# Kernel tuning notes

Hardware: AMD Instinct MI355X
Metric: run time of the kernel (lower is better)

The kernel has to match this reference:

```python
import jax, jax.numpy as jnp
import numpy as np

EMBED_DIM = 1024
HEAD_DIM = 64
B, S = 16, 2048


def setup_inputs() -> dict:
    key = jax.random.key(0)
    ks = jax.random.split(key, 8)
    scale = 1.0 / np.sqrt(EMBED_DIM)
    return {
        "x": jax.random.normal(ks[0], (B, S, EMBED_DIM), dtype=jnp.float32),
        "mask": jax.random.randint(ks[1], (B, S), 0, 2, dtype=jnp.int32),
        "Wq": jax.random.normal(ks[2], (EMBED_DIM, HEAD_DIM), dtype=jnp.float32) * scale,
        "bq": jnp.zeros((HEAD_DIM,), dtype=jnp.float32),
        "Wk": jax.random.normal(ks[3], (EMBED_DIM, HEAD_DIM), dtype=jnp.float32) * scale,
        "bk": jnp.zeros((HEAD_DIM,), dtype=jnp.float32),
        "Wv": jax.random.normal(ks[4], (EMBED_DIM, HEAD_DIM), dtype=jnp.float32) * scale,
        "bv": jnp.zeros((HEAD_DIM,), dtype=jnp.float32),
    }


def reference(x, mask, Wq, bq, Wk, bk, Wv, bv):
    # x: [B,S,E], mask: [B,S] with 0 = masked, 1 = keep
    q = x @ Wq + bq          # [B,S,D]
    k = x @ Wk + bk          # [B,S,D]
    v = x @ Wv + bv          # [B,S,D]
    scores = jnp.einsum("bsd,btd->bst", q, k) / jnp.sqrt(jnp.float32(HEAD_DIM))
    scores = jnp.where(mask[:, None, :] == 0, jnp.float32(-1e9), scores)
    attn = jax.nn.softmax(scores, axis=-1)  # [B,S,S]
    return jnp.einsum("bst,btd->bsd", attn, v)  # [B,S,D]
```

## Files before the change

### kernel.cpp

```cpp
#include <hip/hip_runtime.h>
#include <math.h>

#define EMBED 1024
#define HDIM  64
#define BATCH 16
#define SEQ   2048
#define MTOT  (BATCH*SEQ)
#define NE    (MTOT*HDIM)

typedef _Float16 f16;
typedef __attribute__((ext_vector_type(8))) _Float16 half8;
typedef __attribute__((ext_vector_type(4))) _Float16 half4;
typedef __attribute__((ext_vector_type(4))) float  float4v;

__global__ void wprep_kernel(const float* __restrict__ Wq, const float* __restrict__ Wk,
                             const float* __restrict__ Wv, f16* __restrict__ Wt)
{
    int e = blockIdx.x * 256 + threadIdx.x;
    if (e >= 192 * EMBED) return;
    int gn = e >> 10, k = e & 1023;
    int mat = gn >> 6, n = gn & 63;
    const float* W = (mat == 0) ? Wq : ((mat == 1) ? Wk : Wv);
    Wt[e] = (f16)W[k * HDIM + n];
}

__global__ __launch_bounds__(256)
void qkv_mfma_kernel(const float* __restrict__ X, const f16* __restrict__ Wt,
                     const float* __restrict__ bq, const float* __restrict__ bk, const float* __restrict__ bv,
                     f16* __restrict__ Q, f16* __restrict__ K, f16* __restrict__ Vt)
{
    __shared__ f16 Xs[64 * 72];
    __shared__ f16 Csv[64 * 72];

    const int tid  = threadIdx.x;
    const int wave = tid >> 6;
    const int lane = tid & 63;
    const int quad = lane >> 4;
    const int c16  = lane & 15;
    const int m0   = blockIdx.x * 64;
    const int gnb  = wave * 3;

    float4v acc[4][3];
    #pragma unroll
    for (int mt = 0; mt < 4; ++mt)
        #pragma unroll
        for (int nt = 0; nt < 3; ++nt)
            acc[mt][nt] = (float4v){0.f, 0.f, 0.f, 0.f};

    float4 pf[4];
    #pragma unroll
    for (int i = 0; i < 4; ++i) {
        int c = tid + 256 * i, m = c >> 4, ko = (c & 15) * 4;
        pf[i] = *(const float4*)(X + (size_t)(m0 + m) * EMBED + ko);
    }

    for (int k0 = 0; k0 < EMBED; k0 += 64) {
        half8 bh[2][3];
        #pragma unroll
        for (int ks = 0; ks < 2; ++ks)
            #pragma unroll
            for (int nt = 0; nt < 3; ++nt)
                bh[ks][nt] = *(const half8*)(Wt + (size_t)((gnb + nt) * 16 + c16) * EMBED
                                             + k0 + ks * 32 + quad * 8);

        __syncthreads();
        #pragma unroll
        for (int i = 0; i < 4; ++i) {
            int c = tid + 256 * i, m = c >> 4, ko = (c & 15) * 4;
            half4 h = { (f16)pf[i].x, (f16)pf[i].y, (f16)pf[i].z, (f16)pf[i].w };
            *(half4*)&Xs[m * 72 + ko] = h;
        }
        __syncthreads();

        {
            int k1 = (k0 + 64) & (EMBED - 1);
            #pragma unroll
            for (int i = 0; i < 4; ++i) {
                int c = tid + 256 * i, m = c >> 4, ko = (c & 15) * 4;
                pf[i] = *(const float4*)(X + (size_t)(m0 + m) * EMBED + k1 + ko);
            }
        }

        #pragma unroll
        for (int ks = 0; ks < 2; ++ks) {
            half8 a[4];
            #pragma unroll
            for (int mt = 0; mt < 4; ++mt)
                a[mt] = *(const half8*)&Xs[(mt * 16 + c16) * 72 + ks * 32 + quad * 8];
            #pragma unroll
            for (int mt = 0; mt < 4; ++mt)
                #pragma unroll
                for (int nt = 0; nt < 3; ++nt)
                    acc[mt][nt] = __builtin_amdgcn_mfma_f32_16x16x32_f16(a[mt], bh[ks][nt], acc[mt][nt], 0, 0, 0);
        }
    }

    float bb[3];
    #pragma unroll
    for (int nt = 0; nt < 3; ++nt) {
        int gn = (gnb + nt) * 16 + c16, mat = gn >> 6, cn = gn & 63;
        bb[nt] = ((mat == 0) ? bq : ((mat == 1) ? bk : bv))[cn];
    }

    #pragma unroll
    for (int mt = 0; mt < 4; ++mt)
        #pragma unroll
        for (int nt = 0; nt < 3; ++nt) {
            int gn = (gnb + nt) * 16 + c16, mat = gn >> 6, cn = gn & 63;
            if (mat < 2) {
                f16* O = mat ? K : Q;
                #pragma unroll
                for (int r = 0; r < 4; ++r)
                    O[(size_t)(m0 + mt * 16 + quad * 4 + r) * HDIM + cn] =
                        (f16)(acc[mt][nt][r] + bb[nt]);
            }
        }

    __syncthreads();
    #pragma unroll
    for (int mt = 0; mt < 4; ++mt)
        #pragma unroll
        for (int nt = 0; nt < 3; ++nt) {
            int gn = (gnb + nt) * 16 + c16, mat = gn >> 6, cn = gn & 63;
            if (mat == 2) {
                #pragma unroll
                for (int r = 0; r < 4; ++r)
                    Csv[cn * 72 + mt * 16 + quad * 4 + r] = (f16)(acc[mt][nt][r] + bb[nt]);
            }
        }
    __syncthreads();
    {
        int d = tid >> 2, ms = (tid & 3) * 16;
        #pragma unroll
        for (int j = 0; j < 2; ++j)
            *(half8*)(Vt + (size_t)d * MTOT + m0 + ms + 8 * j) =
                *(const half8*)&Csv[d * 72 + ms + 8 * j];
    }
}

__global__ __launch_bounds__(256)
void attn_mfma_kernel(const f16* __restrict__ Q, const f16* __restrict__ K,
                      const f16* __restrict__ Vt, const int* __restrict__ mask,
                      float* __restrict__ out)
{
    __shared__ f16 Ks[64 * 72];
    __shared__ f16 Vs[64 * 72];
    __shared__ f16 Ps[4 * 16 * 72];
    __shared__ int maskS[64];

    const int tid  = threadIdx.x;
    const int wave = tid >> 6;
    const int lane = tid & 63;
    const int quad = lane >> 4;
    const int c16  = lane & 15;
    const int b    = blockIdx.y;
    const int s0   = blockIdx.x * 64;
    const int q0   = s0 + wave * 16;

    const size_t qrow = (size_t)(b * SEQ + q0 + c16) * HDIM;
    half8 qa0 = *(const half8*)(Q + qrow + quad * 8);
    half8 qa1 = *(const half8*)(Q + qrow + 32 + quad * 8);

    const half8 ones = { (f16)1.f, (f16)1.f, (f16)1.f, (f16)1.f,
                         (f16)1.f, (f16)1.f, (f16)1.f, (f16)1.f };

    float4v O[4];
    #pragma unroll
    for (int dt = 0; dt < 4; ++dt) O[dt] = (float4v){0.f, 0.f, 0.f, 0.f};
    float4v lacc = (float4v){0.f, 0.f, 0.f, 0.f};

    const size_t kbase = (size_t)b * SEQ * HDIM;
    const int vcol0 = b * SEQ;
    const int pbase = wave * 16 * 72;

    half8 pfK[2], pfV[2];
    int mreg;
    #pragma unroll
    for (int i = 0; i < 2; ++i) {
        int c = tid + 256 * i, j = c >> 3, o = (c & 7) * 8;
        pfK[i] = *(const half8*)(K  + kbase + (size_t)j * HDIM + o);
        pfV[i] = *(const half8*)(Vt + (size_t)j * MTOT + vcol0 + o);
    }
    mreg = mask[b * SEQ + (tid & 63)];

    for (int t0 = 0; t0 < SEQ; t0 += 64) {
        __syncthreads();
        #pragma unroll
        for (int i = 0; i < 2; ++i) {
            int c = tid + 256 * i, j = c >> 3, o = (c & 7) * 8;
            *(half8*)&Ks[j * 72 + o] = pfK[i];
            *(half8*)&Vs[j * 72 + o] = pfV[i];
        }
        if (tid < 64) maskS[tid] = mreg;
        __syncthreads();

        {
            int t1 = (t0 + 64) & (SEQ - 1);
            #pragma unroll
            for (int i = 0; i < 2; ++i) {
                int c = tid + 256 * i, j = c >> 3, o = (c & 7) * 8;
                pfK[i] = *(const half8*)(K  + kbase + (size_t)(t1 + j) * HDIM + o);
                pfV[i] = *(const half8*)(Vt + (size_t)j * MTOT + vcol0 + t1 + o);
            }
            mreg = mask[b * SEQ + t1 + (tid & 63)];
        }

        float4v s[4];
        #pragma unroll
        for (int nt = 0; nt < 4; ++nt) {
            const int krow = (nt * 16 + c16) * 72;
            half8 kh0 = *(const half8*)&Ks[krow + quad * 8];
            half8 kh1 = *(const half8*)&Ks[krow + 32 + quad * 8];
            float4v a = (float4v){0.f, 0.f, 0.f, 0.f};
            a = __builtin_amdgcn_mfma_f32_16x16x32_f16(qa0, kh0, a, 0, 0, 0);
            a = __builtin_amdgcn_mfma_f32_16x16x32_f16(qa1, kh1, a, 0, 0, 0);
            s[nt] = a;
        }

        #pragma unroll
        for (int nt = 0; nt < 4; ++nt) {
            int mk = maskS[nt * 16 + c16];
            #pragma unroll
            for (int r = 0; r < 4; ++r) {
                float t = fmaf(s[nt][r], 0.125f, -6.0f);
                t = mk ? t : -1e30f;
                Ps[pbase + (quad * 4 + r) * 72 + nt * 16 + c16] = (f16)__expf(t);
            }
        }

        const int prow = pbase + c16 * 72;
        half8 pa0 = *(const half8*)&Ps[prow + quad * 8];
        half8 pa1 = *(const half8*)&Ps[prow + 32 + quad * 8];
        lacc = __builtin_amdgcn_mfma_f32_16x16x32_f16(pa0, ones, lacc, 0, 0, 0);
        lacc = __builtin_amdgcn_mfma_f32_16x16x32_f16(pa1, ones, lacc, 0, 0, 0);
        #pragma unroll
        for (int dt = 0; dt < 4; ++dt) {
            const int vrow = (dt * 16 + c16) * 72;
            half8 vh0 = *(const half8*)&Vs[vrow + quad * 8];
            half8 vh1 = *(const half8*)&Vs[vrow + 32 + quad * 8];
            O[dt] = __builtin_amdgcn_mfma_f32_16x16x32_f16(pa0, vh0, O[dt], 0, 0, 0);
            O[dt] = __builtin_amdgcn_mfma_f32_16x16x32_f16(pa1, vh1, O[dt], 0, 0, 0);
        }
    }

    #pragma unroll
    for (int r = 0; r < 4; ++r) {
        float inv = 1.0f / lacc[r];
        size_t orow = (size_t)(b * SEQ + q0 + quad * 4 + r) * HDIM;
        #pragma unroll
        for (int dt = 0; dt < 4; ++dt)
            out[orow + dt * 16 + c16] = O[dt][r] * inv;
    }
}

extern "C" void kernel_launch(void* const* d_in, const int* in_sizes, int n_in,
                              void* d_out, int out_size, void* d_ws, size_t ws_size,
                              hipStream_t stream) {
    const float* x    = (const float*)d_in[0];
    const int*   mask = (const int*)  d_in[1];
    const float* Wq   = (const float*)d_in[2];
    const float* bq   = (const float*)d_in[3];
    const float* Wk   = (const float*)d_in[4];
    const float* bk   = (const float*)d_in[5];
    const float* Wv   = (const float*)d_in[6];
    const float* bv   = (const float*)d_in[7];
    float* out = (float*)d_out;

    f16* Qf = (f16*)d_ws;
    f16* Kf = Qf + (size_t)NE;
    f16* Vt = Kf + (size_t)NE;
    f16* Wt = Vt + (size_t)NE;

    wprep_kernel<<<dim3(768), dim3(256), 0, stream>>>(Wq, Wk, Wv, Wt);

    qkv_mfma_kernel<<<dim3(MTOT / 64), dim3(256), 0, stream>>>(
        x, Wt, bq, bk, bv, Qf, Kf, Vt);

    attn_mfma_kernel<<<dim3(SEQ / 64, BATCH), dim3(256), 0, stream>>>(
        Qf, Kf, Vt, mask, out);
}
```

Baseline: 261.6 us.

## Store K/V in MFMA fragment layout, split KV across blocks, add combine pass

The QKV kernel now writes K and V directly in per-lane MFMA fragment order, so the attention kernel loads operands straight from global memory into registers and no longer stages them through LDS with barriers. The X tile in the projection is double-buffered with a two-stage register prefetch, which drops one barrier per step. Attention splits the key range in two along a new grid dimension, and a new combine kernel sums the unnormalized partials and divides by the summed denominators. The exp is computed with exp2f using a pre-scaled constant. In exchange there is an extra launch plus fp32 partial-output traffic, and the attention kernel relies on global and L2 latency instead of shared-memory reuse.

```diff
diff --git a/kernel.cpp b/kernel.cpp
--- a/kernel.cpp
+++ b/kernel.cpp
@@ -27,9 +27,9 @@
 __global__ __launch_bounds__(256)
 void qkv_mfma_kernel(const float* __restrict__ X, const f16* __restrict__ Wt,
                      const float* __restrict__ bq, const float* __restrict__ bk, const float* __restrict__ bv,
-                     f16* __restrict__ Q, f16* __restrict__ K, f16* __restrict__ Vt)
-{
-    __shared__ f16 Xs[64 * 72];
+                     f16* __restrict__ Q, f16* __restrict__ Kf, f16* __restrict__ Vf)
+{
+    __shared__ f16 Xs[2][64 * 72];
     __shared__ f16 Csv[64 * 72];
 
     const int tid  = threadIdx.x;
@@ -47,53 +47,58 @@
         for (int nt = 0; nt < 3; ++nt)
             acc[mt][nt] = (float4v){0.f, 0.f, 0.f, 0.f};
 
-    float4 pf[4];
+    float4 pfA[4], pfB[4];
     #pragma unroll
     for (int i = 0; i < 4; ++i) {
         int c = tid + 256 * i, m = c >> 4, ko = (c & 15) * 4;
-        pf[i] = *(const float4*)(X + (size_t)(m0 + m) * EMBED + ko);
-    }
-
-    for (int k0 = 0; k0 < EMBED; k0 += 64) {
-        half8 bh[2][3];
-        #pragma unroll
-        for (int ks = 0; ks < 2; ++ks)
-            #pragma unroll
-            for (int nt = 0; nt < 3; ++nt)
-                bh[ks][nt] = *(const half8*)(Wt + (size_t)((gnb + nt) * 16 + c16) * EMBED
-                                             + k0 + ks * 32 + quad * 8);
-
-        __syncthreads();
-        #pragma unroll
-        for (int i = 0; i < 4; ++i) {
-            int c = tid + 256 * i, m = c >> 4, ko = (c & 15) * 4;
-            half4 h = { (f16)pf[i].x, (f16)pf[i].y, (f16)pf[i].z, (f16)pf[i].w };
-            *(half4*)&Xs[m * 72 + ko] = h;
-        }
-        __syncthreads();
-
-        {
-            int k1 = (k0 + 64) & (EMBED - 1);
-            #pragma unroll
-            for (int i = 0; i < 4; ++i) {
-                int c = tid + 256 * i, m = c >> 4, ko = (c & 15) * 4;
-                pf[i] = *(const float4*)(X + (size_t)(m0 + m) * EMBED + k1 + ko);
-            }
-        }
-
-        #pragma unroll
-        for (int ks = 0; ks < 2; ++ks) {
-            half8 a[4];
-            #pragma unroll
-            for (int mt = 0; mt < 4; ++mt)
-                a[mt] = *(const half8*)&Xs[(mt * 16 + c16) * 72 + ks * 32 + quad * 8];
-            #pragma unroll
-            for (int mt = 0; mt < 4; ++mt)
-                #pragma unroll
-                for (int nt = 0; nt < 3; ++nt)
-                    acc[mt][nt] = __builtin_amdgcn_mfma_f32_16x16x32_f16(a[mt], bh[ks][nt], acc[mt][nt], 0, 0, 0);
-        }
-    }
+        pfA[i] = *(const float4*)(X + (size_t)(m0 + m) * EMBED + ko);
+        pfB[i] = *(const float4*)(X + (size_t)(m0 + m) * EMBED + 64 + ko);
+    }
+
+#define QKV_STEP(PF, BUF, T)                                                      \
+    {                                                                             \
+        const int k0s = (T) * 64;                                                 \
+        half8 bh[2][3];                                                           \
+        _Pragma("unroll")                                                         \
+        for (int ks = 0; ks < 2; ++ks)                                            \
+            _Pragma("unroll")                                                     \
+            for (int nt = 0; nt < 3; ++nt)                                        \
+                bh[ks][nt] = *(const half8*)(Wt + (size_t)((gnb + nt) * 16 + c16) * EMBED \
+                                             + k0s + ks * 32 + quad * 8);         \
+        _Pragma("unroll")                                                         \
+        for (int i = 0; i < 4; ++i) {                                             \
+            int c = tid + 256 * i, m = c >> 4, ko = (c & 15) * 4;                 \
+            half4 h = { (f16)PF[i].x, (f16)PF[i].y, (f16)PF[i].z, (f16)PF[i].w }; \
+            *(half4*)&Xs[BUF][m * 72 + ko] = h;                                   \
+        }                                                                         \
+        __syncthreads();                                                          \
+        {                                                                         \
+            int k2 = (((T) + 2) & 15) * 64;                                       \
+            _Pragma("unroll")                                                     \
+            for (int i = 0; i < 4; ++i) {                                         \
+                int c = tid + 256 * i, m = c >> 4, ko = (c & 15) * 4;             \
+                PF[i] = *(const float4*)(X + (size_t)(m0 + m) * EMBED + k2 + ko); \
+            }                                                                     \
+        }                                                                         \
+        _Pragma("unroll")                                                         \
+        for (int ks = 0; ks < 2; ++ks) {                                          \
+            half8 a[4];                                                           \
+            _Pragma("unroll")                                                     \
+            for (int mt = 0; mt < 4; ++mt)                                        \
+                a[mt] = *(const half8*)&Xs[BUF][(mt * 16 + c16) * 72 + ks * 32 + quad * 8]; \
+            _Pragma("unroll")                                                     \
+            for (int mt = 0; mt < 4; ++mt)                                        \
+                _Pragma("unroll")                                                 \
+                for (int nt = 0; nt < 3; ++nt)                                    \
+                    acc[mt][nt] = __builtin_amdgcn_mfma_f32_16x16x32_f16(a[mt], bh[ks][nt], acc[mt][nt], 0, 0, 0); \
+        }                                                                         \
+    }
+
+    for (int t = 0; t < 16; t += 2) {
+        QKV_STEP(pfA, 0, t)
+        QKV_STEP(pfB, 1, t + 1)
+    }
+#undef QKV_STEP
 
     float bb[3];
     #pragma unroll
@@ -107,12 +112,20 @@
         #pragma unroll
         for (int nt = 0; nt < 3; ++nt) {
             int gn = (gnb + nt) * 16 + c16, mat = gn >> 6, cn = gn & 63;
-            if (mat < 2) {
-                f16* O = mat ? K : Q;
+            if (mat == 0) {
                 #pragma unroll
                 for (int r = 0; r < 4; ++r)
-                    O[(size_t)(m0 + mt * 16 + quad * 4 + r) * HDIM + cn] =
+                    Q[(size_t)(m0 + mt * 16 + quad * 4 + r) * HDIM + cn] =
                         (f16)(acc[mt][nt][r] + bb[nt]);
+            } else if (mat == 1) {
+                int ks = cn >> 5, q2 = (cn >> 3) & 3, dd = cn & 7;
+                int jt = (m0 >> 4) + mt;
+                #pragma unroll
+                for (int r = 0; r < 4; ++r) {
+                    int lanep = q2 * 16 + (quad * 4 + r);
+                    int idx = (jt * 2 + ks) * 512 + lanep * 8 + dd;
+                    Kf[idx] = (f16)(acc[mt][nt][r] + bb[nt]);
+                }
             }
         }
 
@@ -130,23 +143,26 @@
         }
     __syncthreads();
     {
-        int d = tid >> 2, ms = (tid & 3) * 16;
-        #pragma unroll
-        for (int j = 0; j < 2; ++j)
-            *(half8*)(Vt + (size_t)d * MTOT + m0 + ms + 8 * j) =
-                *(const half8*)&Csv[d * 72 + ms + 8 * j];
+        int c   = tid >> 5;
+        int s2  = tid & 31;
+        int jvl = c >> 2, dt = c & 3;
+        int fragg = ((m0 >> 5) + jvl) * 4 + dt;
+        #pragma unroll
+        for (int sub = 0; sub < 2; ++sub) {
+            int lp = s2 * 2 + sub;
+            int qp = lp >> 4, cp = lp & 15;
+            half8 v = *(const half8*)&Csv[(dt * 16 + cp) * 72 + jvl * 32 + qp * 8];
+            *(half8*)(Vf + (size_t)fragg * 512 + lp * 8) = v;
+        }
     }
 }
 
 __global__ __launch_bounds__(256)
-void attn_mfma_kernel(const f16* __restrict__ Q, const f16* __restrict__ K,
-                      const f16* __restrict__ Vt, const int* __restrict__ mask,
-                      float* __restrict__ out)
-{
-    __shared__ f16 Ks[64 * 72];
-    __shared__ f16 Vs[64 * 72];
+void attn_mfma_kernel(const f16* __restrict__ Q, const f16* __restrict__ Kf,
+                      const f16* __restrict__ Vf, const int* __restrict__ mask,
+                      float* __restrict__ Opart, float* __restrict__ lpart)
+{
     __shared__ f16 Ps[4 * 16 * 72];
-    __shared__ int maskS[64];
 
     const int tid  = threadIdx.x;
     const int wave = tid >> 6;
@@ -154,8 +170,8 @@
     const int quad = lane >> 4;
     const int c16  = lane & 15;
     const int b    = blockIdx.y;
-    const int s0   = blockIdx.x * 64;
-    const int q0   = s0 + wave * 16;
+    const int kvh  = blockIdx.z;
+    const int q0   = blockIdx.x * 64 + wave * 16;
 
     const size_t qrow = (size_t)(b * SEQ + q0 + c16) * HDIM;
     half8 qa0 = *(const half8*)(Q + qrow + quad * 8);
@@ -169,88 +185,80 @@
     for (int dt = 0; dt < 4; ++dt) O[dt] = (float4v){0.f, 0.f, 0.f, 0.f};
     float4v lacc = (float4v){0.f, 0.f, 0.f, 0.f};
 
-    const size_t kbase = (size_t)b * SEQ * HDIM;
-    const int vcol0 = b * SEQ;
     const int pbase = wave * 16 * 72;
-
-    half8 pfK[2], pfV[2];
-    int mreg;
-    #pragma unroll
-    for (int i = 0; i < 2; ++i) {
-        int c = tid + 256 * i, j = c >> 3, o = (c & 7) * 8;
-        pfK[i] = *(const half8*)(K  + kbase + (size_t)j * HDIM + o);
-        pfV[i] = *(const half8*)(Vt + (size_t)j * MTOT + vcol0 + o);
-    }
-    mreg = mask[b * SEQ + (tid & 63)];
-
-    for (int t0 = 0; t0 < SEQ; t0 += 64) {
-        __syncthreads();
-        #pragma unroll
-        for (int i = 0; i < 2; ++i) {
-            int c = tid + 256 * i, j = c >> 3, o = (c & 7) * 8;
-            *(half8*)&Ks[j * 72 + o] = pfK[i];
-            *(half8*)&Vs[j * 72 + o] = pfV[i];
-        }
-        if (tid < 64) maskS[tid] = mreg;
-        __syncthreads();
-
-        {
-            int t1 = (t0 + 64) & (SEQ - 1);
+    const int prow  = pbase + c16 * 72;
+    const int t_beg = kvh * (SEQ / 2);
+    const int t_end = t_beg + (SEQ / 2);
+
+    for (int t0 = t_beg; t0 < t_end; t0 += 64) {
+        const size_t fb = (size_t)(b * SEQ + t0) * 64;
+
+        float4v s[4];
+        #pragma unroll
+        for (int nt = 0; nt < 4; ++nt) {
+            half8 k0 = *(const half8*)(Kf + fb + nt * 1024 + lane * 8);
+            half8 k1 = *(const half8*)(Kf + fb + nt * 1024 + 512 + lane * 8);
+            float4v a = (float4v){0.f, 0.f, 0.f, 0.f};
+            a = __builtin_amdgcn_mfma_f32_16x16x32_f16(qa0, k0, a, 0, 0, 0);
+            a = __builtin_amdgcn_mfma_f32_16x16x32_f16(qa1, k1, a, 0, 0, 0);
+            s[nt] = a;
+        }
+
+        half8 vf[4][2];
+        #pragma unroll
+        for (int dt = 0; dt < 4; ++dt)
             #pragma unroll
-            for (int i = 0; i < 2; ++i) {
-                int c = tid + 256 * i, j = c >> 3, o = (c & 7) * 8;
-                pfK[i] = *(const half8*)(K  + kbase + (size_t)(t1 + j) * HDIM + o);
-                pfV[i] = *(const half8*)(Vt + (size_t)j * MTOT + vcol0 + t1 + o);
-            }
-            mreg = mask[b * SEQ + t1 + (tid & 63)];
-        }
-
-        float4v s[4];
+            for (int ks = 0; ks < 2; ++ks)
+                vf[dt][ks] = *(const half8*)(Vf + fb + ks * 2048 + dt * 512 + lane * 8);
+
+        const int* mrow = mask + b * SEQ + t0;
         #pragma unroll
         for (int nt = 0; nt < 4; ++nt) {
-            const int krow = (nt * 16 + c16) * 72;
-            half8 kh0 = *(const half8*)&Ks[krow + quad * 8];
-            half8 kh1 = *(const half8*)&Ks[krow + 32 + quad * 8];
-            float4v a = (float4v){0.f, 0.f, 0.f, 0.f};
-            a = __builtin_amdgcn_mfma_f32_16x16x32_f16(qa0, kh0, a, 0, 0, 0);
-            a = __builtin_amdgcn_mfma_f32_16x16x32_f16(qa1, kh1, a, 0, 0, 0);
-            s[nt] = a;
-        }
-
-        #pragma unroll
-        for (int nt = 0; nt < 4; ++nt) {
-            int mk = maskS[nt * 16 + c16];
+            int mk = mrow[nt * 16 + c16];
             #pragma unroll
             for (int r = 0; r < 4; ++r) {
-                float t = fmaf(s[nt][r], 0.125f, -6.0f);
+                float t = fmaf(s[nt][r], 0.18033688011112042f, -8.656170245333781f);
                 t = mk ? t : -1e30f;
-                Ps[pbase + (quad * 4 + r) * 72 + nt * 16 + c16] = (f16)__expf(t);
+                Ps[pbase + (quad * 4 + r) * 72 + nt * 16 + c16] = (f16)exp2f(t);
             }
         }
 
-        const int prow = pbase + c16 * 72;
         half8 pa0 = *(const half8*)&Ps[prow + quad * 8];
         half8 pa1 = *(const half8*)&Ps[prow + 32 + quad * 8];
         lacc = __builtin_amdgcn_mfma_f32_16x16x32_f16(pa0, ones, lacc, 0, 0, 0);
         lacc = __builtin_amdgcn_mfma_f32_16x16x32_f16(pa1, ones, lacc, 0, 0, 0);
         #pragma unroll
         for (int dt = 0; dt < 4; ++dt) {
-            const int vrow = (dt * 16 + c16) * 72;
-            half8 vh0 = *(const half8*)&Vs[vrow + quad * 8];
-            half8 vh1 = *(const half8*)&Vs[vrow + 32 + quad * 8];
-            O[dt] = __builtin_amdgcn_mfma_f32_16x16x32_f16(pa0, vh0, O[dt], 0, 0, 0);
-            O[dt] = __builtin_amdgcn_mfma_f32_16x16x32_f16(pa1, vh1, O[dt], 0, 0, 0);
+            O[dt] = __builtin_amdgcn_mfma_f32_16x16x32_f16(pa0, vf[dt][0], O[dt], 0, 0, 0);
+            O[dt] = __builtin_amdgcn_mfma_f32_16x16x32_f16(pa1, vf[dt][1], O[dt], 0, 0, 0);
         }
     }
 
     #pragma unroll
     for (int r = 0; r < 4; ++r) {
-        float inv = 1.0f / lacc[r];
-        size_t orow = (size_t)(b * SEQ + q0 + quad * 4 + r) * HDIM;
+        size_t orow = (size_t)kvh * NE + (size_t)(b * SEQ + q0 + quad * 4 + r) * HDIM;
         #pragma unroll
         for (int dt = 0; dt < 4; ++dt)
-            out[orow + dt * 16 + c16] = O[dt][r] * inv;
-    }
+            Opart[orow + dt * 16 + c16] = O[dt][r];
+        if (c16 == 0)
+            lpart[kvh * MTOT + b * SEQ + q0 + quad * 4 + r] = lacc[r];
+    }
+}
+
+__global__ __launch_bounds__(256)
+void combine_kernel(const float* __restrict__ Opart, const float* __restrict__ lpart,
+                    float* __restrict__ out)
+{
+    int gid = blockIdx.x * 256 + threadIdx.x;
+    int row = gid >> 4;
+    const float4* O0 = (const float4*)Opart;
+    const float4* O1 = (const float4*)(Opart + (size_t)NE);
+    float4 a = O0[gid], c = O1[gid];
+    float inv = 1.0f / (lpart[row] + lpart[MTOT + row]);
+    float4 o;
+    o.x = (a.x + c.x) * inv; o.y = (a.y + c.y) * inv;
+    o.z = (a.z + c.z) * inv; o.w = (a.w + c.w) * inv;
+    ((float4*)out)[gid] = o;
 }
 
 extern "C" void kernel_launch(void* const* d_in, const int* in_sizes, int n_in,
@@ -268,14 +276,18 @@
 
     f16* Qf = (f16*)d_ws;
     f16* Kf = Qf + (size_t)NE;
-    f16* Vt = Kf + (size_t)NE;
-    f16* Wt = Vt + (size_t)NE;
+    f16* Vf = Kf + (size_t)NE;
+    f16* Wt = Vf + (size_t)NE;
+    float* Opart = (float*)(Wt + 192 * EMBED);
+    float* lpart = Opart + 2 * (size_t)NE;
 
     wprep_kernel<<<dim3(768), dim3(256), 0, stream>>>(Wq, Wk, Wv, Wt);
 
     qkv_mfma_kernel<<<dim3(MTOT / 64), dim3(256), 0, stream>>>(
-        x, Wt, bq, bk, bv, Qf, Kf, Vt);
-
-    attn_mfma_kernel<<<dim3(SEQ / 64, BATCH), dim3(256), 0, stream>>>(
-        Qf, Kf, Vt, mask, out);
-}
+        x, Wt, bq, bk, bv, Qf, Kf, Vf);
+
+    attn_mfma_kernel<<<dim3(SEQ / 64, BATCH, 2), dim3(256), 0, stream>>>(
+        Qf, Kf, Vf, mask, Opart, lpart);
+
+    combine_kernel<<<dim3(NE / 4 / 256), dim3(256), 0, stream>>>(Opart, lpart, out);
+}
```

Measured after the change: 265.1 us. No clear change (+1.3%).
